# Performance work log

Measured on AMD Instinct MI355X. Metric: run time of the kernel, lower is better.

## Reference

```python
import jax, jax.numpy as jnp
import numpy as np

P = 512       # protein_dim
D = 512       # drug_dim
N = 2000      # neighbors per layer
E = 300000    # binding edges per layer
ND = 100000   # total drugs
BASELINE = 6.0
LN_EPS = 1e-5


def setup_inputs() -> dict:
    key = jax.random.key(0)
    ks = jax.random.split(key, 24)
    inp = {
        "target_features": jax.random.normal(ks[0], (P,), jnp.float32),
        "form_features": jax.random.normal(ks[1], (N, P), jnp.float32),
        "role_features": jax.random.normal(ks[2], (N, P), jnp.float32),
        "form_neighbors": jnp.arange(N, dtype=jnp.int64) if jax.config.jax_enable_x64 else jnp.arange(N, dtype=jnp.int32),
        "role_neighbors": jnp.arange(N, dtype=jnp.int32),
        "form_binds_ei": jax.random.randint(ks[3], (2, E), 0, N, jnp.int32),
        "form_binds_y": jax.random.uniform(ks[4], (E,), jnp.float32) * 8.0 + 2.0,
        "role_binds_ei": jax.random.randint(ks[5], (2, E), 0, N, jnp.int32),
        "role_binds_y": jax.random.uniform(ks[6], (E,), jnp.float32) * 8.0 + 2.0,
        "drug_features": jax.random.normal(ks[7], (ND, D), jnp.float32),
    }
    inp["form_neighbors"] = jnp.arange(N, dtype=jnp.int32)
    attn_in = P * 2 + 16
    s1 = 1.0 / np.sqrt(attn_in)
    s2 = 1.0 / np.sqrt(64)
    sd = 1.0 / np.sqrt(D)
    sp = 1.0 / np.sqrt(P)
    inp["layer_emb"] = jax.random.normal(ks[8], (2, 16), jnp.float32)
    inp["W1"] = jax.random.uniform(ks[9], (attn_in, 64), jnp.float32, -s1, s1)
    inp["b1"] = jax.random.uniform(ks[10], (64,), jnp.float32, -s1, s1)
    inp["W2"] = jax.random.uniform(ks[11], (64, 1), jnp.float32, -s2, s2)
    inp["b2"] = jax.random.uniform(ks[12], (1,), jnp.float32, -s2, s2)
    inp["Wi1"] = jax.random.uniform(ks[13], (D, P), jnp.float32, -sd, sd)
    inp["bi1"] = jax.random.uniform(ks[14], (P,), jnp.float32, -sd, sd)
    inp["prelu_alpha"] = jnp.array(0.25, jnp.float32)
    inp["Wi2"] = jax.random.uniform(ks[15], (P, P), jnp.float32, -sp, sp)
    inp["bi2"] = jax.random.uniform(ks[16], (P,), jnp.float32, -sp, sp)
    inp["ln_gamma"] = jnp.ones((P,), jnp.float32)
    inp["ln_beta"] = jnp.zeros((P,), jnp.float32)
    return inp


def _pref_vectors(neighbor_ids, ei, y, drug_features):
    # Vectorized form of the per-neighbor masked gather-sum:
    # for each edge, find its neighbor slot (neighbor_ids is sorted);
    # edges whose src id is not a neighbor get zero weight.
    n = neighbor_ids.shape[0]
    pos = jnp.clip(jnp.searchsorted(neighbor_ids, ei[0]), 0, n - 1)
    valid = neighbor_ids[pos] == ei[0]
    w = jnp.where(valid, y - BASELINE, 0.0)              # [E]
    contrib = drug_features[ei[1]] * w[:, None]          # [E, D] gather (memory-bound)
    return jax.ops.segment_sum(contrib, pos, num_segments=n)  # [N, D]


def _attention(z_target, z_neighbors, l_vec, W1, b1, W2, b2):
    n = z_neighbors.shape[0]
    inp = jnp.concatenate(
        [jnp.broadcast_to(z_target, (n, z_target.shape[0])),
         z_neighbors,
         jnp.broadcast_to(l_vec, (n, l_vec.shape[0]))], axis=-1)  # [N, 2P+16]
    h = inp @ W1 + b1
    h = jnp.where(h > 0, h, 0.2 * h)  # LeakyReLU(0.2)
    return h @ W2 + b2                # [N, 1]


def reference(target_features, form_features, role_features, form_neighbors,
              role_neighbors, form_binds_ei, form_binds_y, role_binds_ei,
              role_binds_y, drug_features, layer_emb, W1, b1, W2, b2,
              Wi1, bi1, prelu_alpha, Wi2, bi2, ln_gamma, ln_beta):
    form_msgs = _pref_vectors(form_neighbors, form_binds_ei, form_binds_y, drug_features)
    role_msgs = _pref_vectors(role_neighbors, role_binds_ei, role_binds_y, drug_features)

    form_attn = _attention(target_features, form_features, layer_emb[0], W1, b1, W2, b2)
    role_attn = _attention(target_features, role_features, layer_emb[1], W1, b1, W2, b2)

    all_msgs = jnp.concatenate([form_msgs, role_msgs], axis=0)   # [2N, D]
    all_attn = jnp.concatenate([form_attn, role_attn], axis=0)   # [2N, 1]
    attn_weights = jax.nn.softmax(all_attn, axis=0)
    v_prior = jnp.sum(attn_weights * all_msgs, axis=0)           # [D]

    h = v_prior @ Wi1 + bi1
    h = jnp.where(h > 0, h, prelu_alpha * h)  # PReLU
    v = h @ Wi2 + bi2                          # [P]

    x = target_features + v
    mu = jnp.mean(x)
    var = jnp.mean(jnp.square(x - mu))
    z_refined = (x - mu) / jnp.sqrt(var + LN_EPS) * ln_gamma + ln_beta
    return (z_refined, form_msgs, role_msgs)
```

## Files before the change

### kernel.cpp

```cpp
#include <hip/hip_runtime.h>
#include <math.h>

static constexpr int PD = 512;
static constexpr float BASEV = 6.0f;
static constexpr int CAP = 320;

__global__ void edge_kernel(const int* __restrict__ ei_f, const float* __restrict__ y_f,
                            const int* __restrict__ ei_r, const float* __restrict__ y_r,
                            const int* __restrict__ nb_f, const int* __restrict__ nb_r,
                            int N, int E, int* __restrict__ cnt,
                            int* __restrict__ sj, float* __restrict__ sw) {
    int i = blockIdx.x * blockDim.x + threadIdx.x;
    if (i >= 2 * E) return;
    bool role = i >= E;
    int e = role ? i - E : i;
    const int* ei0 = role ? ei_r : ei_f;
    const int* ei1 = (role ? ei_r : ei_f) + E;
    int v = ei0[e];
    const int* nb = role ? nb_r : nb_f;
    int lo = 0, hi = N;
    while (lo < hi) { int mid = (lo + hi) >> 1; if (nb[mid] < v) lo = mid + 1; else hi = mid; }
    int pos = lo < N ? lo : N - 1;
    if (nb[pos] != v) return;
    int s = role ? N + pos : pos;
    int j = ei1[e];
    float w = (role ? y_r[e] : y_f[e]) - BASEV;
    int slot = atomicAdd(&cnt[s], 1);
    if (slot < CAP) { sj[s * CAP + slot] = j; sw[s * CAP + slot] = w; }
}

__global__ __launch_bounds__(128) void accum_kernel(const int* __restrict__ cnt,
                                                    const int* __restrict__ sj,
                                                    const float* __restrict__ sw,
                                                    const float* __restrict__ drug,
                                                    float* __restrict__ msgs) {
    int b = blockIdx.x;
    int t = threadIdx.x;
    int n = cnt[b]; n = n < CAP ? n : CAP;
    const int* sjb = sj + b * CAP;
    const float* swb = sw + b * CAP;
    float4 acc = make_float4(0.f, 0.f, 0.f, 0.f);
    int k = 0;
    for (; k + 3 < n; k += 4) {
        int j0 = sjb[k], j1 = sjb[k + 1], j2 = sjb[k + 2], j3 = sjb[k + 3];
        float w0 = swb[k], w1 = swb[k + 1], w2 = swb[k + 2], w3 = swb[k + 3];
        float4 d0 = ((const float4*)(drug + (size_t)j0 * PD))[t];
        float4 d1 = ((const float4*)(drug + (size_t)j1 * PD))[t];
        float4 d2 = ((const float4*)(drug + (size_t)j2 * PD))[t];
        float4 d3 = ((const float4*)(drug + (size_t)j3 * PD))[t];
        acc.x += w0 * d0.x; acc.y += w0 * d0.y; acc.z += w0 * d0.z; acc.w += w0 * d0.w;
        acc.x += w1 * d1.x; acc.y += w1 * d1.y; acc.z += w1 * d1.z; acc.w += w1 * d1.w;
        acc.x += w2 * d2.x; acc.y += w2 * d2.y; acc.z += w2 * d2.z; acc.w += w2 * d2.w;
        acc.x += w3 * d3.x; acc.y += w3 * d3.y; acc.z += w3 * d3.z; acc.w += w3 * d3.w;
    }
    for (; k < n; k++) {
        int j0 = sjb[k];
        float w0 = swb[k];
        float4 d0 = ((const float4*)(drug + (size_t)j0 * PD))[t];
        acc.x += w0 * d0.x; acc.y += w0 * d0.y; acc.z += w0 * d0.z; acc.w += w0 * d0.w;
    }
    ((float4*)(msgs + (size_t)b * PD))[t] = acc;
}

__global__ void attn_const_kernel(const float* __restrict__ target, const float* __restrict__ lemb,
                                  const float* __restrict__ W1, const float* __restrict__ b1,
                                  float* __restrict__ cbuf) {
    int l = blockIdx.x, j = threadIdx.x;
    float c = b1[j];
    for (int p = 0; p < PD; p++) c += target[p] * W1[p * 64 + j];
    for (int q = 0; q < 16; q++) c += lemb[l * 16 + q] * W1[(2 * PD + q) * 64 + j];
    cbuf[l * 64 + j] = c;
}

__global__ __launch_bounds__(256) void attn_kernel(const float* __restrict__ formF,
                                                   const float* __restrict__ roleF,
                                                   const float* __restrict__ W1,
                                                   const float* __restrict__ W2,
                                                   const float* __restrict__ b2,
                                                   const float* __restrict__ cbuf,
                                                   int N, float* __restrict__ logits) {
    int wave = threadIdx.x >> 6, lane = threadIdx.x & 63;
    int s = blockIdx.x * 4 + wave;
    if (s >= 2 * N) return;
    int rl = s >= N ? 1 : 0;
    const float* z = rl ? roleF + (size_t)(s - N) * PD : formF + (size_t)s * PD;
    const float* w1p = W1 + PD * 64 + lane;
    float h0 = cbuf[rl * 64 + lane], h1 = 0.f, h2 = 0.f, h3 = 0.f;
    for (int p = 0; p < PD; p += 4) {
        h0 += z[p + 0] * w1p[(size_t)(p + 0) * 64];
        h1 += z[p + 1] * w1p[(size_t)(p + 1) * 64];
        h2 += z[p + 2] * w1p[(size_t)(p + 2) * 64];
        h3 += z[p + 3] * w1p[(size_t)(p + 3) * 64];
    }
    float h = (h0 + h1) + (h2 + h3);
    h = h > 0.f ? h : 0.2f * h;
    float v = h * W2[lane];
#pragma unroll
    for (int off = 32; off > 0; off >>= 1) v += __shfl_down(v, off, 64);
    if (lane == 0) logits[s] = v + b2[0];
}

__global__ __launch_bounds__(128) void vprior_kernel(const float* __restrict__ logits,
                                                     const float* __restrict__ msgs,
                                                     int nseg, float* __restrict__ v_prior) {
    __shared__ float red[128];
    int t = threadIdx.x;
    float m = -1e30f;
    for (int s = t; s < nseg; s += 128) m = fmaxf(m, logits[s]);
    red[t] = m; __syncthreads();
    for (int o = 64; o > 0; o >>= 1) { if (t < o) red[t] = fmaxf(red[t], red[t + o]); __syncthreads(); }
    m = red[0]; __syncthreads();
    float sum = 0.f;
    for (int s = t; s < nseg; s += 128) sum += expf(logits[s] - m);
    red[t] = sum; __syncthreads();
    for (int o = 64; o > 0; o >>= 1) { if (t < o) red[t] += red[t + o]; __syncthreads(); }
    float inv = 1.f / red[0];

    float4 acc = make_float4(0.f, 0.f, 0.f, 0.f);
    for (int s = blockIdx.x; s < nseg; s += gridDim.x) {
        float w = expf(logits[s] - m) * inv;
        float4 d = ((const float4*)(msgs + (size_t)s * PD))[t];
        acc.x += w * d.x; acc.y += w * d.y; acc.z += w * d.z; acc.w += w * d.w;
    }
    atomicAdd(&v_prior[4 * t + 0], acc.x);
    atomicAdd(&v_prior[4 * t + 1], acc.y);
    atomicAdd(&v_prior[4 * t + 2], acc.z);
    atomicAdd(&v_prior[4 * t + 3], acc.w);
}

__global__ __launch_bounds__(256) void mv1_kernel(const float* __restrict__ v_prior,
                                                  const float* __restrict__ Wi1,
                                                  float* __restrict__ h) {
    int b = blockIdx.x;
    int t = threadIdx.x;
    float2 acc = make_float2(0.f, 0.f);
    int d0 = b * 16;
    for (int d = d0; d < d0 + 16; d++) {
        float vd = v_prior[d];
        float2 w = ((const float2*)(Wi1 + (size_t)d * PD))[t];
        acc.x += vd * w.x; acc.y += vd * w.y;
    }
    atomicAdd(&h[2 * t + 0], acc.x);
    atomicAdd(&h[2 * t + 1], acc.y);
}

__global__ __launch_bounds__(256) void mv2_kernel(const float* __restrict__ h,
                                                  const float* __restrict__ bi1,
                                                  const float* __restrict__ alpha_p,
                                                  const float* __restrict__ Wi2,
                                                  float* __restrict__ v) {
    int b = blockIdx.x;
    int t = threadIdx.x;
    float alpha = alpha_p[0];
    float2 acc = make_float2(0.f, 0.f);
    int q0 = b * 16;
    for (int q = q0; q < q0 + 16; q++) {
        float hq = h[q] + bi1[q];
        hq = hq > 0.f ? hq : alpha * hq;
        float2 w = ((const float2*)(Wi2 + (size_t)q * PD))[t];
        acc.x += hq * w.x; acc.y += hq * w.y;
    }
    atomicAdd(&v[2 * t + 0], acc.x);
    atomicAdd(&v[2 * t + 1], acc.y);
}

__global__ __launch_bounds__(512) void final_kernel(const float* __restrict__ target,
                                                    const float* __restrict__ v,
                                                    const float* __restrict__ bi2,
                                                    const float* __restrict__ gamma,
                                                    const float* __restrict__ beta,
                                                    float* __restrict__ out) {
    __shared__ float red[512];
    int t = threadIdx.x;
    float x = target[t] + v[t] + bi2[t];
    red[t] = x; __syncthreads();
    for (int o = 256; o > 0; o >>= 1) { if (t < o) red[t] += red[t + o]; __syncthreads(); }
    float mu = red[0] * (1.f / 512.f);
    __syncthreads();
    float dx = x - mu;
    red[t] = dx * dx; __syncthreads();
    for (int o = 256; o > 0; o >>= 1) { if (t < o) red[t] += red[t + o]; __syncthreads(); }
    float var = red[0] * (1.f / 512.f);
    out[t] = dx * (1.f / sqrtf(var + 1e-5f)) * gamma[t] + beta[t];
}

extern "C" void kernel_launch(void* const* d_in, const int* in_sizes, int n_in,
                              void* d_out, int out_size, void* d_ws, size_t ws_size,
                              hipStream_t stream) {
    const float* target = (const float*)d_in[0];
    const float* formF  = (const float*)d_in[1];
    const float* roleF  = (const float*)d_in[2];
    const int*   nb_f   = (const int*)d_in[3];
    const int*   nb_r   = (const int*)d_in[4];
    const int*   ei_f   = (const int*)d_in[5];
    const float* y_f    = (const float*)d_in[6];
    const int*   ei_r   = (const int*)d_in[7];
    const float* y_r    = (const float*)d_in[8];
    const float* drug   = (const float*)d_in[9];
    const float* lemb   = (const float*)d_in[10];
    const float* W1     = (const float*)d_in[11];
    const float* b1     = (const float*)d_in[12];
    const float* W2     = (const float*)d_in[13];
    const float* b2     = (const float*)d_in[14];
    const float* Wi1    = (const float*)d_in[15];
    const float* bi1    = (const float*)d_in[16];
    const float* alpha  = (const float*)d_in[17];
    const float* Wi2    = (const float*)d_in[18];
    const float* bi2    = (const float*)d_in[19];
    const float* gamma  = (const float*)d_in[20];
    const float* beta   = (const float*)d_in[21];

    int N = in_sizes[3];
    int E = in_sizes[5] / 2;
    int nseg = 2 * N;

    int* ws = (int*)d_ws;
    int*   cnt     = ws + 0;
    float* v_prior = (float*)(ws + 4096);
    float* hbuf    = (float*)(ws + 4608);
    float* vbuf    = (float*)(ws + 5120);
    float* cbuf    = (float*)(ws + 5632);
    float* logits  = (float*)(ws + 5760);
    int*   sj      = ws + 9856;
    float* sw      = (float*)(sj + 4096 * CAP);

    float* out  = (float*)d_out;
    float* msgs = out + PD;

    hipMemsetAsync(ws, 0, 5632 * sizeof(int), stream);

    int nb2E = (2 * E + 255) / 256;
    edge_kernel<<<nb2E, 256, 0, stream>>>(ei_f, y_f, ei_r, y_r, nb_f, nb_r, N, E, cnt, sj, sw);
    attn_const_kernel<<<2, 64, 0, stream>>>(target, lemb, W1, b1, cbuf);
    attn_kernel<<<(nseg + 3) / 4, 256, 0, stream>>>(formF, roleF, W1, W2, b2, cbuf, N, logits);
    accum_kernel<<<nseg, 128, 0, stream>>>(cnt, sj, sw, drug, msgs);
    vprior_kernel<<<64, 128, 0, stream>>>(logits, msgs, nseg, v_prior);
    mv1_kernel<<<32, 256, 0, stream>>>(v_prior, Wi1, hbuf);
    mv2_kernel<<<32, 256, 0, stream>>>(hbuf, bi1, alpha, Wi2, vbuf);
    final_kernel<<<1, 512, 0, stream>>>(target, vbuf, bi2, gamma, beta, out);
}
```

Before: 500.4 us.

## Fuse edge binning and attention into one front kernel with packed bins

Merges the edge-binning, attention-constant and attention-logit kernels into a single launch, with block ranges assigned to each role. Each attention wave now handles 8 rows, so every W1 column load is reused across rows, and it computes the per-layer constant itself instead of reading it from a separate kernel's buffer. Bin entries are packed as int2 (index, weight) to halve the scattered stores and loads, and the accumulation loop is unrolled to 8 gathers. The cost is redundant constant computation per wave and higher register pressure in the fused kernel.

```diff
diff --git a/kernel.cpp b/kernel.cpp
--- a/kernel.cpp
+++ b/kernel.cpp
@@ -5,99 +5,128 @@
 static constexpr float BASEV = 6.0f;
 static constexpr int CAP = 320;
 
-__global__ void edge_kernel(const int* __restrict__ ei_f, const float* __restrict__ y_f,
-                            const int* __restrict__ ei_r, const float* __restrict__ y_r,
-                            const int* __restrict__ nb_f, const int* __restrict__ nb_r,
-                            int N, int E, int* __restrict__ cnt,
-                            int* __restrict__ sj, float* __restrict__ sw) {
-    int i = blockIdx.x * blockDim.x + threadIdx.x;
-    if (i >= 2 * E) return;
-    bool role = i >= E;
-    int e = role ? i - E : i;
-    const int* ei0 = role ? ei_r : ei_f;
-    const int* ei1 = (role ? ei_r : ei_f) + E;
-    int v = ei0[e];
-    const int* nb = role ? nb_r : nb_f;
-    int lo = 0, hi = N;
-    while (lo < hi) { int mid = (lo + hi) >> 1; if (nb[mid] < v) lo = mid + 1; else hi = mid; }
-    int pos = lo < N ? lo : N - 1;
-    if (nb[pos] != v) return;
-    int s = role ? N + pos : pos;
-    int j = ei1[e];
-    float w = (role ? y_r[e] : y_f[e]) - BASEV;
-    int slot = atomicAdd(&cnt[s], 1);
-    if (slot < CAP) { sj[s * CAP + slot] = j; sw[s * CAP + slot] = w; }
+__global__ __launch_bounds__(256) void front_kernel(
+    const int* __restrict__ ei_f, const float* __restrict__ y_f,
+    const int* __restrict__ ei_r, const float* __restrict__ y_r,
+    const int* __restrict__ nb_f, const int* __restrict__ nb_r,
+    const float* __restrict__ target, const float* __restrict__ formF,
+    const float* __restrict__ roleF, const float* __restrict__ lemb,
+    const float* __restrict__ W1, const float* __restrict__ b1,
+    const float* __restrict__ W2, const float* __restrict__ b2,
+    int N, int E, int eb,
+    int* __restrict__ cnt, int2* __restrict__ bins,
+    float* __restrict__ logits) {
+    int b = blockIdx.x;
+    if (b < eb) {
+        int i = b * 256 + threadIdx.x;
+        if (i >= 2 * E) return;
+        bool role = i >= E;
+        int e = role ? i - E : i;
+        const int* ei0 = role ? ei_r : ei_f;
+        const int* ei1 = (role ? ei_r : ei_f) + E;
+        int v = ei0[e];
+        const int* nb = role ? nb_r : nb_f;
+        int lo = 0, hi = N;
+        while (lo < hi) { int mid = (lo + hi) >> 1; if (nb[mid] < v) lo = mid + 1; else hi = mid; }
+        int pos = lo < N ? lo : N - 1;
+        if (nb[pos] != v) return;
+        int s = role ? N + pos : pos;
+        float w = (role ? y_r[e] : y_f[e]) - BASEV;
+        int slot = atomicAdd(&cnt[s], 1);
+        if (slot < CAP) bins[(size_t)s * CAP + slot] = make_int2(ei1[e], __float_as_int(w));
+    } else {
+        int wave = threadIdx.x >> 6, lane = threadIdx.x & 63;
+        int r0 = ((b - eb) * 4 + wave) * 8;
+        int nseg = 2 * N;
+        if (r0 >= nseg) return;
+        const float* W1t = W1 + lane;
+        float c = b1[lane];
+        const float4* t4 = (const float4*)target;
+        for (int p = 0; p < PD; p += 4) {
+            float4 tv = t4[p >> 2];
+            c += tv.x * W1t[(size_t)(p + 0) * 64] + tv.y * W1t[(size_t)(p + 1) * 64]
+               + tv.z * W1t[(size_t)(p + 2) * 64] + tv.w * W1t[(size_t)(p + 3) * 64];
+        }
+        float c0 = c, c1 = c;
+        for (int q = 0; q < 16; q++) {
+            float wq = W1t[(size_t)(2 * PD + q) * 64];
+            c0 += lemb[q] * wq;
+            c1 += lemb[16 + q] * wq;
+        }
+        int nrows = nseg - r0; if (nrows > 8) nrows = 8;
+        const float* z[8];
+        float h[8];
+#pragma unroll
+        for (int r = 0; r < 8; r++) {
+            int rr = r0 + (r < nrows ? r : 0);
+            bool rl = rr >= N;
+            z[r] = rl ? roleF + (size_t)(rr - N) * PD : formF + (size_t)rr * PD;
+            h[r] = rl ? c1 : c0;
+        }
+        const float* W1z = W1 + (size_t)PD * 64 + lane;
+        for (int p = 0; p < PD; p += 4) {
+            float w0 = W1z[(size_t)(p + 0) * 64], w1 = W1z[(size_t)(p + 1) * 64];
+            float w2 = W1z[(size_t)(p + 2) * 64], w3 = W1z[(size_t)(p + 3) * 64];
+#pragma unroll
+            for (int r = 0; r < 8; r++) {
+                float4 zv = *(const float4*)(z[r] + p);
+                h[r] += zv.x * w0 + zv.y * w1 + zv.z * w2 + zv.w * w3;
+            }
+        }
+        float w2l = W2[lane];
+#pragma unroll
+        for (int r = 0; r < 8; r++) {
+            float hh = h[r];
+            hh = hh > 0.f ? hh : 0.2f * hh;
+            float vv = hh * w2l;
+#pragma unroll
+            for (int off = 32; off > 0; off >>= 1) vv += __shfl_down(vv, off, 64);
+            if (lane == 0 && r < nrows) logits[r0 + r] = vv + b2[0];
+        }
+    }
 }
 
 __global__ __launch_bounds__(128) void accum_kernel(const int* __restrict__ cnt,
-                                                    const int* __restrict__ sj,
-                                                    const float* __restrict__ sw,
+                                                    const int2* __restrict__ bins,
                                                     const float* __restrict__ drug,
                                                     float* __restrict__ msgs) {
     int b = blockIdx.x;
     int t = threadIdx.x;
     int n = cnt[b]; n = n < CAP ? n : CAP;
-    const int* sjb = sj + b * CAP;
-    const float* swb = sw + b * CAP;
+    const int2* bb = bins + (size_t)b * CAP;
     float4 acc = make_float4(0.f, 0.f, 0.f, 0.f);
     int k = 0;
-    for (; k + 3 < n; k += 4) {
-        int j0 = sjb[k], j1 = sjb[k + 1], j2 = sjb[k + 2], j3 = sjb[k + 3];
-        float w0 = swb[k], w1 = swb[k + 1], w2 = swb[k + 2], w3 = swb[k + 3];
-        float4 d0 = ((const float4*)(drug + (size_t)j0 * PD))[t];
-        float4 d1 = ((const float4*)(drug + (size_t)j1 * PD))[t];
-        float4 d2 = ((const float4*)(drug + (size_t)j2 * PD))[t];
-        float4 d3 = ((const float4*)(drug + (size_t)j3 * PD))[t];
+    for (; k + 7 < n; k += 8) {
+        int2 e0 = bb[k + 0], e1 = bb[k + 1], e2 = bb[k + 2], e3 = bb[k + 3];
+        int2 e4 = bb[k + 4], e5 = bb[k + 5], e6 = bb[k + 6], e7 = bb[k + 7];
+        float4 d0 = ((const float4*)(drug + (size_t)e0.x * PD))[t];
+        float4 d1 = ((const float4*)(drug + (size_t)e1.x * PD))[t];
+        float4 d2 = ((const float4*)(drug + (size_t)e2.x * PD))[t];
+        float4 d3 = ((const float4*)(drug + (size_t)e3.x * PD))[t];
+        float4 d4 = ((const float4*)(drug + (size_t)e4.x * PD))[t];
+        float4 d5 = ((const float4*)(drug + (size_t)e5.x * PD))[t];
+        float4 d6 = ((const float4*)(drug + (size_t)e6.x * PD))[t];
+        float4 d7 = ((const float4*)(drug + (size_t)e7.x * PD))[t];
+        float w0 = __int_as_float(e0.y), w1 = __int_as_float(e1.y);
+        float w2 = __int_as_float(e2.y), w3 = __int_as_float(e3.y);
+        float w4 = __int_as_float(e4.y), w5 = __int_as_float(e5.y);
+        float w6 = __int_as_float(e6.y), w7 = __int_as_float(e7.y);
         acc.x += w0 * d0.x; acc.y += w0 * d0.y; acc.z += w0 * d0.z; acc.w += w0 * d0.w;
         acc.x += w1 * d1.x; acc.y += w1 * d1.y; acc.z += w1 * d1.z; acc.w += w1 * d1.w;
         acc.x += w2 * d2.x; acc.y += w2 * d2.y; acc.z += w2 * d2.z; acc.w += w2 * d2.w;
         acc.x += w3 * d3.x; acc.y += w3 * d3.y; acc.z += w3 * d3.z; acc.w += w3 * d3.w;
+        acc.x += w4 * d4.x; acc.y += w4 * d4.y; acc.z += w4 * d4.z; acc.w += w4 * d4.w;
+        acc.x += w5 * d5.x; acc.y += w5 * d5.y; acc.z += w5 * d5.z; acc.w += w5 * d5.w;
+        acc.x += w6 * d6.x; acc.y += w6 * d6.y; acc.z += w6 * d6.z; acc.w += w6 * d6.w;
+        acc.x += w7 * d7.x; acc.y += w7 * d7.y; acc.z += w7 * d7.z; acc.w += w7 * d7.w;
     }
     for (; k < n; k++) {
-        int j0 = sjb[k];
-        float w0 = swb[k];
-        float4 d0 = ((const float4*)(drug + (size_t)j0 * PD))[t];
+        int2 e0 = bb[k];
+        float w0 = __int_as_float(e0.y);
+        float4 d0 = ((const float4*)(drug + (size_t)e0.x * PD))[t];
         acc.x += w0 * d0.x; acc.y += w0 * d0.y; acc.z += w0 * d0.z; acc.w += w0 * d0.w;
     }
     ((float4*)(msgs + (size_t)b * PD))[t] = acc;
-}
-
-__global__ void attn_const_kernel(const float* __restrict__ target, const float* __restrict__ lemb,
-                                  const float* __restrict__ W1, const float* __restrict__ b1,
-                                  float* __restrict__ cbuf) {
-    int l = blockIdx.x, j = threadIdx.x;
-    float c = b1[j];
-    for (int p = 0; p < PD; p++) c += target[p] * W1[p * 64 + j];
-    for (int q = 0; q < 16; q++) c += lemb[l * 16 + q] * W1[(2 * PD + q) * 64 + j];
-    cbuf[l * 64 + j] = c;
-}
-
-__global__ __launch_bounds__(256) void attn_kernel(const float* __restrict__ formF,
-                                                   const float* __restrict__ roleF,
-                                                   const float* __restrict__ W1,
-                                                   const float* __restrict__ W2,
-                                                   const float* __restrict__ b2,
-                                                   const float* __restrict__ cbuf,
-                                                   int N, float* __restrict__ logits) {
-    int wave = threadIdx.x >> 6, lane = threadIdx.x & 63;
-    int s = blockIdx.x * 4 + wave;
-    if (s >= 2 * N) return;
-    int rl = s >= N ? 1 : 0;
-    const float* z = rl ? roleF + (size_t)(s - N) * PD : formF + (size_t)s * PD;
-    const float* w1p = W1 + PD * 64 + lane;
-    float h0 = cbuf[rl * 64 + lane], h1 = 0.f, h2 = 0.f, h3 = 0.f;
-    for (int p = 0; p < PD; p += 4) {
-        h0 += z[p + 0] * w1p[(size_t)(p + 0) * 64];
-        h1 += z[p + 1] * w1p[(size_t)(p + 1) * 64];
-        h2 += z[p + 2] * w1p[(size_t)(p + 2) * 64];
-        h3 += z[p + 3] * w1p[(size_t)(p + 3) * 64];
-    }
-    float h = (h0 + h1) + (h2 + h3);
-    h = h > 0.f ? h : 0.2f * h;
-    float v = h * W2[lane];
-#pragma unroll
-    for (int off = 32; off > 0; off >>= 1) v += __shfl_down(v, off, 64);
-    if (lane == 0) logits[s] = v + b2[0];
 }
 
 __global__ __launch_bounds__(128) void vprior_kernel(const float* __restrict__ logits,
@@ -219,21 +248,21 @@
     float* v_prior = (float*)(ws + 4096);
     float* hbuf    = (float*)(ws + 4608);
     float* vbuf    = (float*)(ws + 5120);
-    float* cbuf    = (float*)(ws + 5632);
-    float* logits  = (float*)(ws + 5760);
-    int*   sj      = ws + 9856;
-    float* sw      = (float*)(sj + 4096 * CAP);
+    float* logits  = (float*)(ws + 5632);
+    int2*  bins    = (int2*)(ws + 9728);
 
     float* out  = (float*)d_out;
     float* msgs = out + PD;
 
     hipMemsetAsync(ws, 0, 5632 * sizeof(int), stream);
 
-    int nb2E = (2 * E + 255) / 256;
-    edge_kernel<<<nb2E, 256, 0, stream>>>(ei_f, y_f, ei_r, y_r, nb_f, nb_r, N, E, cnt, sj, sw);
-    attn_const_kernel<<<2, 64, 0, stream>>>(target, lemb, W1, b1, cbuf);
-    attn_kernel<<<(nseg + 3) / 4, 256, 0, stream>>>(formF, roleF, W1, W2, b2, cbuf, N, logits);
-    accum_kernel<<<nseg, 128, 0, stream>>>(cnt, sj, sw, drug, msgs);
+    int EB = (2 * E + 255) / 256;
+    int AB = (nseg + 31) / 32;
+    front_kernel<<<EB + AB, 256, 0, stream>>>(ei_f, y_f, ei_r, y_r, nb_f, nb_r,
+                                              target, formF, roleF, lemb,
+                                              W1, b1, W2, b2, N, E, EB,
+                                              cnt, bins, logits);
+    accum_kernel<<<nseg, 128, 0, stream>>>(cnt, bins, drug, msgs);
     vprior_kernel<<<64, 128, 0, stream>>>(logits, msgs, nseg, v_prior);
     mv1_kernel<<<32, 256, 0, stream>>>(v_prior, Wi1, hbuf);
     mv2_kernel<<<32, 256, 0, stream>>>(hbuf, bi1, alpha, Wi2, vbuf);
```

After: 523.5 us. +4.6%, slower.
